# Kernel tuning notes

Measured on AMD Instinct MI355X. Metric: run time of the kernel, lower is better.

## Reference

```python
import jax, jax.numpy as jnp
import numpy as np

N = 20000; DX = 512; DW = 64; DY = 256; M = 320000
DS = DX // 2; DD = DX // 4; DP = DS + DD  # 256, 128, 384
EPS = 1e-9; LN_EPS = 1e-5; SLOPE = 0.05
PNAMES = ['rW1','rb1','rg1','rbt1','rW2','rb2','yW1','yb1','yg1','ybt1','yW2','yb2',
          'iaW1','iab1','iag1','iabt1','iaW2','iab2','cW1','cb1','cg1','cbt1','cW2','cb2']

def _mlp2(h, W1, b1, g, be, W2, b2):
    # Linear -> LayerNorm -> LeakyReLU(0.05) -> Linear  (matches mlp(..., norm='layer'))
    h = h @ W1 + b1
    mu = jnp.mean(h, axis=-1, keepdims=True)
    var = jnp.mean((h - mu) ** 2, axis=-1, keepdims=True)
    h = (h - mu) * jax.lax.rsqrt(var + LN_EPS) * g + be
    h = jnp.where(h >= 0, h, SLOPE * h)
    return h @ W2 + b2

def _m(Pp, n, h):
    return _mlp2(h, Pp[n+'W1'], Pp[n+'b1'], Pp[n+'g1'], Pp[n+'bt1'], Pp[n+'W2'], Pp[n+'b2'])

def _agg(a, b):
    s = a + b
    return jnp.where(s >= 0, s, SLOPE * s)

def _run(x, ei, edge_attr, u_r, u_ia, u_pick, Pp, dec=None):
    """GuoUnpool forward (steps 1a, 2a, 2b). ei: concrete numpy [2,M] int64.
    dec holds concrete sampled decisions; built from the uniforms when None."""
    build = dec is None
    if build:
        dec = {}
    # coalesce (edges are duplicate-free) + lexsort by (src, dst)
    perm = np.argsort(ei[0].astype(np.int64) * N + ei[1].astype(np.int64), kind='stable')
    src, dst = ei[0][perm], ei[1][perm]
    ea = edge_attr[perm]
    # --- step 1a: bernoulli unpool decision per node (I_s = I_u = empty, I_r = all nodes)
    pr = jax.nn.sigmoid(_m(Pp, 'r', x)[:, 0])
    if build:
        dec['choose'] = np.asarray(u_r) < np.asarray(pr)
    choose = dec['choose']
    Iu = np.flatnonzero(choose); Is = np.flatnonzero(~choose)
    logP = jnp.sum(jnp.where(jnp.asarray(choose), jnp.log(pr + EPS), jnp.log(1.0 - pr + EPS)))
    prs = jnp.clip(pr, EPS, 1.0 - EPS)
    ent = -jnp.sum(prs * jnp.log(prs) + (1.0 - prs) * jnp.log(1.0 - prs))
    # --- projections (_ps1_idx = [0:ds+D], _ps2_idx = [0:ds] + [ds+D:ds+2D]) and child embeddings
    ps1 = x[:, :DP]
    ps2 = jnp.concatenate([x[:, :DS], x[:, DS + DD:DS + 2 * DD]], axis=-1)
    y1 = _m(Pp, 'y', ps1)   # [N, dy]; rows at Is give x_static, rows at Iu give x_c1
    y2 = _m(Pp, 'y', ps2)   # rows at Iu give x_c2
    x_out = jnp.concatenate([y1[Is], y1[Iu], y2[Iu]], axis=0)
    # --- step 2a: intra-edge decision for unpooled nodes
    p_ia = jax.nn.sigmoid(_m(Pp, 'ia', _agg(y1[Iu], y2[Iu]))[:, 0])
    if build:
        dec['vc'] = np.asarray(u_ia)[Iu] < np.asarray(p_ia)
    vc = dec['vc']
    logP = logP + jnp.sum(jnp.where(jnp.asarray(vc), jnp.log(p_ia + EPS), jnp.log(1.0 - p_ia + EPS)))
    ps = jnp.clip(p_ia, EPS, 1.0 - EPS)
    ent = ent - jnp.sum(ps * jnp.log(ps) + (1.0 - ps) * jnp.log(1.0 - ps))
    # --- step 2b: categorical neighbor pick for unpooled nodes without intra edge
    if build:
        iun = Iu[~vc]
        par = np.concatenate([src, dst]); nb = np.concatenate([dst, src])
        ek = np.concatenate([np.arange(len(src)), np.arange(len(src))])
        keep = np.zeros(N, dtype=bool); keep[iun] = True
        msk = keep[par]
        par, nb, ek = par[msk], nb[msk], ek[msk]
        o = np.lexsort((nb, par))  # adj lists sorted by neighbor id, grouped by parent
        par, nb, ek = par[o], nb[o], ek[o]
        new = np.r_[True, par[1:] != par[:-1]]
        dec['par'], dec['nb'], dec['ek'] = par, nb, ek
        dec['seg'] = np.cumsum(new) - 1
        dec['starts'] = np.flatnonzero(new)
    par, nb, ek = dec['par'], dec['nb'], dec['ek']
    segn, starts = dec['seg'], dec['starts']
    Pn = len(par); nseg = int(segn[-1]) + 1
    seg = jnp.asarray(segn)
    yagg = _agg(y1, y2)
    feats = jnp.concatenate([yagg[par], ea[ek], x[nb]], axis=-1)  # [Pn, dy+dw+dx]
    scores = _m(Pp, 'c', feats)[:, 0]
    mx = jax.ops.segment_max(scores, seg, num_segments=nseg)
    e = jnp.exp(scores - mx[segn])
    den = jax.ops.segment_sum(e, seg, num_segments=nseg)
    probs = e / den[segn]                      # per-parent softmax over neighbors
    if build:
        # multinomial pick via inverse CDF on the provided per-parent uniform
        p_np = np.asarray(probs).astype(np.float64)
        cum = np.cumsum(p_np)
        base = np.concatenate([[0.0], cum])[starts]
        cumw = cum - base[segn]
        useg = np.asarray(u_pick)[par[starts]][segn]
        cand = np.where(cumw > useg, np.arange(Pn), Pn)
        pick = np.minimum.reduceat(cand, starts)
        last = np.r_[starts[1:] - 1, Pn - 1]
        dec['pick'] = np.minimum(pick, last)
    pick = dec['pick']
    logP = logP + jnp.sum(jnp.log(jnp.clip(probs[pick], EPS, None)))
    pc = jnp.clip(probs, EPS, None)
    ent = ent - jnp.sum(pc * jnp.log(pc))
    return (x_out, logP, ent), dec

def _init_params(key):
    Pp = {}
    specs = [('r', DX, max(1, DX // 2), 1), ('y', DP, 128, DY), ('ia', DY, 128, 1), ('c', DY + DW + DX, 128, 1)]
    ks = jax.random.split(key, len(specs))
    for (n, a, h, o), k in zip(specs, ks):
        k1, k2 = jax.random.split(k)
        Pp[n+'W1'] = jax.random.normal(k1, (a, h), jnp.float32) / np.sqrt(a)
        Pp[n+'b1'] = jnp.zeros((h,), jnp.float32)
        Pp[n+'g1'] = jnp.ones((h,), jnp.float32)
        Pp[n+'bt1'] = jnp.zeros((h,), jnp.float32)
        Pp[n+'W2'] = jax.random.normal(k2, (h, o), jnp.float32) / np.sqrt(h)
        Pp[n+'b2'] = jnp.zeros((o,), jnp.float32)
    return Pp

def setup_inputs() -> dict:
    key = jax.random.key(0)
    k = jax.random.split(key, 6)
    x = jax.random.normal(k[0], (N, DX), jnp.float32)
    rng = np.random.default_rng(0)
    ns = int(M * 1.5)
    s = rng.integers(0, N, ns); d = rng.integers(0, N, ns)
    ok = s != d; s, d = s[ok], d[ok]
    _, ui = np.unique(s.astype(np.int64) * N + d, return_index=True)  # duplicate-free (coalesced)
    sel = rng.permutation(ui)[:M]
    edge_index = jnp.asarray(np.stack([s[sel], d[sel]]).astype(np.int64))
    inp = {
        'x': x,
        'edge_index': edge_index,
        'edge_attr': 0.5 * jax.random.normal(k[1], (M, DW), jnp.float32),
        'u_r': jax.random.uniform(k[2], (N,), jnp.float32),
        'u_ia': jax.random.uniform(k[3], (N,), jnp.float32),
        'u_pick': jax.random.uniform(k[4], (N,), jnp.float32),
    }
    inp.update(_init_params(k[5]))
    return inp

def reference(x, edge_index, edge_attr, u_r, u_ia, u_pick,
              rW1, rb1, rg1, rbt1, rW2, rb2,
              yW1, yb1, yg1, ybt1, yW2, yb2,
              iaW1, iab1, iag1, iabt1, iaW2, iab2,
              cW1, cb1, cg1, cbt1, cW2, cb2):
    Pp = dict(zip(PNAMES, (rW1, rb1, rg1, rbt1, rW2, rb2, yW1, yb1, yg1, ybt1, yW2, yb2,
                           iaW1, iab1, iag1, iabt1, iaW2, iab2, cW1, cb1, cg1, cbt1, cW2, cb2)))
    out, _ = _run(x, np.asarray(edge_index), edge_attr, u_r, u_ia, u_pick, Pp)
    return out
```

## Files before the change

### kernel.cpp

```cpp
#include <hip/hip_runtime.h>
#include <math.h>

#define KN 20000
#define KM 320000

typedef __attribute__((ext_vector_type(8))) short bf16x8;
typedef __attribute__((ext_vector_type(4))) float f32x4;

__device__ __forceinline__ ushort f2bf(float f){
  union{float f; unsigned u;} a; a.f=f;
  unsigned r = a.u + 0x7FFFu + ((a.u>>16)&1u);
  return (ushort)(r>>16);
}
__device__ __forceinline__ float bf2f(ushort u){
  union{unsigned u; float f;} a; a.u=((unsigned)u)<<16; return a.f;
}

__device__ __forceinline__ void blk_add2(double lp, double en, double* acc, double* sh){
#pragma unroll
  for (int o=32;o;o>>=1){ lp+=__shfl_xor(lp,o,64); en+=__shfl_xor(en,o,64); }
  int w=threadIdx.x>>6;
  if ((threadIdx.x&63)==0){ sh[2*w]=lp; sh[2*w+1]=en; }
  __syncthreads();
  if (threadIdx.x==0){
    double L=0,E=0; int nw=(blockDim.x+63)>>6;
    for (int i=0;i<nw;i++){L+=sh[2*i];E+=sh[2*i+1];}
    atomicAdd(&acc[0],L); atomicAdd(&acc[1],E);
  }
  __syncthreads();
}

__global__ void k_init(int* __restrict__ deg,int* __restrict__ fill,int* __restrict__ keep,
                       int* __restrict__ counters,double* __restrict__ acc){
  int i=blockIdx.x*blockDim.x+threadIdx.x;
  if (i<KN){ deg[i]=0; fill[i]=0; keep[i]=0; }
  if (i<8) counters[i]=0;
  if (i<2) acc[i]=0.0;
}

__global__ __launch_bounds__(256) void k_cvt2(const float* __restrict__ src,
    ushort* __restrict__ hi, ushort* __restrict__ lo, int n8){
  int i=blockIdx.x*256+threadIdx.x;
  if (i<n8){
    const float* s=src+(size_t)i*8;
    union{ushort u[8]; uint4 v;} oh, ol;
#pragma unroll
    for (int j=0;j<8;j++){
      float v=s[j];
      ushort h=f2bf(v);
      oh.u[j]=h;
      ol.u[j]=f2bf(v-bf2f(h));
    }
    *(uint4*)(hi+(size_t)i*8)=oh.v;
    *(uint4*)(lo+(size_t)i*8)=ol.v;
  }
}

__global__ __launch_bounds__(256) void k_prep_w1d(const float* __restrict__ W1, double* __restrict__ w1d){
  int i=blockIdx.x*256+threadIdx.x;
  if (i<512*256) w1d[i]=(double)W1[i];
}
__global__ __launch_bounds__(256) void k_prep_wr2(const float* __restrict__ W1,
    ushort* __restrict__ Wrt_hi, ushort* __restrict__ Wrt_lo){
  int i=blockIdx.x*256+threadIdx.x;
  if (i<512*256){
    int n=i&255, k=i>>8;
    float wv=W1[(size_t)k*256+n];
    ushort h=f2bf(wv);
    int kt=k>>5, kc=(k>>3)&3, j=k&7;
    size_t dst=(((size_t)kt*1024)+(size_t)kc*256+(size_t)n)*8+j;
    Wrt_hi[dst]=h;
    Wrt_lo[dst]=f2bf(wv-bf2f(h));
  }
}

#define RFLAG_TAU 3e-4f
__global__ __launch_bounds__(512) void k_rmlp_fast2(const float* __restrict__ x,
    const ushort* __restrict__ x_hi,const ushort* __restrict__ x_lo,
    const ushort* __restrict__ Wrt_hi,const ushort* __restrict__ Wrt_lo,
    const double* __restrict__ w1d,
    const float* __restrict__ b1,const float* __restrict__ g1,
    const float* __restrict__ bt1,const float* __restrict__ W2,const float* __restrict__ b2,
    const float* __restrict__ u_r, float* __restrict__ pr, int* __restrict__ choose){
  __shared__ __align__(16) ushort Bl[2][2][8192];
  __shared__ float psum[64][2], pvar[64][2], pdot[64][2];
  __shared__ int flagsh[64];
  __shared__ double dsh[256];
  int t=threadIdx.x;
  int w=t>>6, l=t&63;
  int lr=l&15, lk=l>>4;
  int rg=w>>1, ch=w&1;
  int row0=blockIdx.x*64;
  if (t<64) flagsh[t]=0;
  int q0=t*2, q1=t*2+1;
  f32x4 acc[8];
#pragma unroll
  for (int c=0;c<8;c++) acc[c]=(f32x4){0,0,0,0};
  int rowA=row0+rg*16+lr; if (rowA>=KN) rowA=KN-1;
  const ushort* ah=x_hi+(size_t)rowA*512;
  const ushort* al=x_lo+(size_t)rowA*512;
  bf16x8 nh0=*(const bf16x8*)(Wrt_hi+q0*8);
  bf16x8 nh1=*(const bf16x8*)(Wrt_hi+q1*8);
  bf16x8 nl0=*(const bf16x8*)(Wrt_lo+q0*8);
  bf16x8 nl1=*(const bf16x8*)(Wrt_lo+q1*8);
  *(bf16x8*)&Bl[0][0][q0*8]=nh0; *(bf16x8*)&Bl[0][0][q1*8]=nh1;
  *(bf16x8*)&Bl[0][1][q0*8]=nl0; *(bf16x8*)&Bl[0][1][q1*8]=nl1;
  nh0=*(const bf16x8*)(Wrt_hi+8192+q0*8);
  nh1=*(const bf16x8*)(Wrt_hi+8192+q1*8);
  nl0=*(const bf16x8*)(Wrt_lo+8192+q0*8);
  nl1=*(const bf16x8*)(Wrt_lo+8192+q1*8);
  bf16x8 a_h0=*(const bf16x8*)(ah+0*32+lk*8), a_l0=*(const bf16x8*)(al+0*32+lk*8);
  bf16x8 a_h1=*(const bf16x8*)(ah+1*32+lk*8), a_l1=*(const bf16x8*)(al+1*32+lk*8);
  bf16x8 a_h2=*(const bf16x8*)(ah+2*32+lk*8), a_l2=*(const bf16x8*)(al+2*32+lk*8);
  bf16x8 a_h3=*(const bf16x8*)(ah+3*32+lk*8), a_l3=*(const bf16x8*)(al+3*32+lk*8);
  __syncthreads();
#define RBODY(KT,AH,AL) { \
    const int cur_=(KT)&1, nxt_=cur_^1; \
    if ((KT)<15){ \
      *(bf16x8*)&Bl[nxt_][0][q0*8]=nh0; *(bf16x8*)&Bl[nxt_][0][q1*8]=nh1; \
      *(bf16x8*)&Bl[nxt_][1][q0*8]=nl0; *(bf16x8*)&Bl[nxt_][1][q1*8]=nl1; \
      if ((KT)<14){ \
        size_t so_=(size_t)((KT)+2)*8192; \
        nh0=*(const bf16x8*)(Wrt_hi+so_+q0*8); nh1=*(const bf16x8*)(Wrt_hi+so_+q1*8); \
// ... 111 lines not shown
      for (int o=32;o;o>>=1) dot+=__shfl_xor(dot,o,64);
      if (t==0){
        double p=1.0/(1.0+exp(-(dot+(double)b2[0])));
        float pf=(float)p;
        pr[n]=pf;
        choose[n]=(u_r[n]<pf)?1:0;
      }
    }
    __syncthreads();
  }
}

__global__ __launch_bounds__(1024) void k_scan_choose(const int* __restrict__ choose,int* __restrict__ excl,
                                                      int* __restrict__ iu,int* __restrict__ counters){
  __shared__ int wsum[16], woff[16];
  const int CH=(KN+1023)/1024;
  int t=threadIdx.x, lane=t&63, wid=t>>6;
  int base=t*CH;
  int s=0;
  for (int i=0;i<CH;i++){int idx=base+i; if (idx<KN) s+=choose[idx];}
  int inc=s;
  for (int o=1;o<64;o<<=1){ int v=__shfl_up(inc,o,64); if (lane>=o) inc+=v; }
  if (lane==63) wsum[wid]=inc;
  __syncthreads();
  if (t==0){ int r=0; for (int i=0;i<16;i++){ woff[i]=r; r+=wsum[i]; } counters[2]=r; }
  __syncthreads();
  int ex=woff[wid]+inc-s;
  for (int i=0;i<CH;i++){
    int idx=base+i;
    if (idx<KN){ int c=choose[idx]; excl[idx]=ex; if (c) iu[ex]=idx; ex+=c; }
  }
}

__global__ void k_prep_w1yt(const float* __restrict__ W1, ushort* __restrict__ W1yt){
  int i=blockIdx.x*256+threadIdx.x;
  if (i<384*128){
    int n=i&127, k=i>>7;
    W1yt[(size_t)n*384+k]=f2bf(W1[(size_t)k*128+n]);
  }
}
__global__ void k_prep_w2yt(const float* __restrict__ W2, ushort* __restrict__ W2yt){
  int i=blockIdx.x*256+threadIdx.x;
  if (i<128*256){
    int n=i&255, k=i>>8;
    W2yt[(size_t)n*128+k]=f2bf(W2[(size_t)k*256+n]);
  }
}

#define YEXTP 261
__global__ __launch_bounds__(256) void k_ymlp_v2(const ushort* __restrict__ x_bf,
    const ushort* __restrict__ W1yt,const float* __restrict__ b1,const float* __restrict__ g1,
    const float* __restrict__ bt1,const ushort* __restrict__ W2yt,const float* __restrict__ b2,
    const int* __restrict__ choose,const int* __restrict__ excl,int cnt,
    float* __restrict__ yagg_f,ushort* __restrict__ yagg_bf,
    float* __restrict__ out){
  __shared__ __align__(16) char smem[16896+8704];
  float*  hf  =(float*)smem;
  float*  yext=(float*)smem;
  ushort* hb  =(ushort*)(smem+16896);
  int t=threadIdx.x;
  int w=t>>6, l=t&63;
  int lr=l&15, lk=l>>4;
  int md=w&1, kh=w>>1;
  int row0=blockIdx.x*16;
  f32x4 acc[8];
#pragma unroll
  for (int c=0;c<8;c++) acc[c]=(f32x4){0,0,0,0};
  const ushort* xr=x_bf+(size_t)(row0+lr)*512;
#pragma unroll
  for (int kt=0;kt<6;kt++){
    int k0=kh*192+kt*32+lk*8;
    int ks=(md && k0>=256)? k0+128 : k0;
    bf16x8 a=*(const bf16x8*)(xr+ks);
#pragma unroll
    for (int c=0;c<8;c++){
      bf16x8 b=*(const bf16x8*)(W1yt+(size_t)(c*16+lr)*384+k0);
      acc[c]=__builtin_amdgcn_mfma_f32_16x16x32_bf16(a,b,acc[c],0,0,0);
    }
  }
  if (kh==0){
#pragma unroll
    for (int i=0;i<4;i++){
      int row=lk*4+i;
#pragma unroll
      for (int c=0;c<8;c++) hf[((size_t)md*16+row)*132+c*16+lr]=acc[c][i];
    }
  }
  __syncthreads();
  if (kh==1){
    float b1v[8],g1v[8],btv[8];
#pragma unroll
    for (int c=0;c<8;c++){ int col=c*16+lr; b1v[c]=b1[col]; g1v[c]=g1[col]; btv[c]=bt1[col]; }
#pragma unroll
    for (int i=0;i<4;i++){
      int row=lk*4+i;
      float hv[8]; float s=0.f;
#pragma unroll
      for (int c=0;c<8;c++){ hv[c]=acc[c][i]+hf[((size_t)md*16+row)*132+c*16+lr]+b1v[c]; s+=hv[c]; }
#pragma unroll
      for (int o=8;o;o>>=1) s+=__shfl_xor(s,o,64);
      float mu=s*(1.0f/128.0f);
      float v=0.f;
#pragma unroll
      for (int c=0;c<8;c++){ float d=hv[c]-mu; v+=d*d; }
#pragma unroll
      for (int o=8;o;o>>=1) v+=__shfl_xor(v,o,64);
      float rs=1.0f/sqrtf(v*(1.0f/128.0f)+1e-5f);
      ushort* hrow=hb+((size_t)md*16+row)*136;
#pragma unroll
      for (int c=0;c<8;c++){
        float hn=(hv[c]-mu)*rs*g1v[c]+btv[c];
        hn=hn>=0.f?hn:0.05f*hn;
        hrow[c*16+lr]=f2bf(hn);
      }
    }
  }
  __syncthreads();
  f32x4 acc2[8];
#pragma unroll
  for (int c=0;c<8;c++) acc2[c]=(f32x4){0,0,0,0};
  const ushort* ha=hb+((size_t)md*16+lr)*136;
#pragma unroll
  for (int kt=0;kt<4;kt++){
    bf16x8 a=*(const bf16x8*)(ha+kt*32+lk*8);
#pragma unroll
    for (int c=0;c<8;c++){
      bf16x8 b=*(const bf16x8*)(W2yt+(size_t)(kh*128+c*16+lr)*128+kt*32+lk*8);
      acc2[c]=__builtin_amdgcn_mfma_f32_16x16x32_bf16(a,b,acc2[c],0,0,0);
    }
  }
  float b2v[8];
#pragma unroll
  for (int c=0;c<8;c++) b2v[c]=b2[kh*128+c*16+lr];
  if (md==0){
#pragma unroll
    for (int i=0;i<4;i++){
      int row=lk*4+i;
#pragma unroll
      for (int c=0;c<8;c++) yext[(size_t)row*YEXTP+kh*128+c*16+lr]=acc2[c][i]+b2v[c];
    }
  }
  __syncthreads();
  if (md==0){
#pragma unroll
    for (int i=0;i<4;i++){
      int row=lk*4+i, n=row0+row;
      int cch=choose[n], ex=excl[n];
      int r1 = cch? (KN-cnt)+ex : n-ex;
      if (r1>=0 && r1<KN+cnt){
        float* orow=out+(size_t)r1*256+kh*128;
#pragma unroll
        for (int c=0;c<8;c++) orow[c*16+lr]=acc2[c][i]+b2v[c];
      }
    }
  } else {
#pragma unroll
    for (int i=0;i<4;i++){
      int row=lk*4+i, n=row0+row;
      int cch=choose[n], ex=excl[n];
      size_t base=(size_t)n*256+kh*128;
#pragma unroll
      for (int c=0;c<8;c++){
        int colk=c*16+lr;
        float v2=acc2[c][i]+b2v[c];
        float v1=yext[(size_t)row*YEXTP+kh*128+colk];
        float ga=v1+v2; ga=ga>=0.f?ga:0.05f*ga;
        yagg_f[base+colk]=ga;
        yagg_bf[base+colk]=f2bf(ga);
        if (cch){ int r2=KN+ex; if (r2<KN+cnt) out[(size_t)r2*256+kh*128+colk]=v2; }
      }
    }
  }
}

__global__ __launch_bounds__(256) void k_node_term(const float* __restrict__ pr,const int* __restrict__ choose,
                                                   double* __restrict__ acc){
  __shared__ double sh[8];
  int i=blockIdx.x*256+threadIdx.x;
  double lp=0,en=0;
  if (i<KN){
    double p=(double)pr[i];
    lp = choose[i]? log(p+1e-9) : log(1.0-p+1e-9);
    double ps=fmin(fmax(p,1e-9),1.0-1e-9);
    en = -(ps*log(ps)+(1.0-ps)*log(1.0-ps));
  }
  blk_add2(lp,en,acc,sh);
}

__global__ __launch_bounds__(128) void k_ia(const float* __restrict__ yagg_f,
    const int* __restrict__ iu,const float* __restrict__ u_ia,
    const float* __restrict__ W1,const float* __restrict__ b1,const float* __restrict__ g1,
    const float* __restrict__ bt1,const float* __restrict__ W2,const float* __restrict__ b2,
    float* __restrict__ p_ia,int* __restrict__ vc,int* __restrict__ keep,double* __restrict__ acc,int cnt){
  __shared__ float insh[8][256];
  __shared__ float hsh[8][128];
  __shared__ double sh[8];
  int t=threadIdx.x;
  int row0=blockIdx.x*8;
  for (int i=t;i<8*256;i+=128){
    int r=i>>8,k=i&255;
    int row=row0+r;
    if (row<cnt){
      unsigned n=(unsigned)iu[row];
      if (n<KN) insh[r][k]=yagg_f[(size_t)n*256+k];
      else insh[r][k]=0.f;
    }
  }
  __syncthreads();
  float accv[8]; float bb=b1[t];
#pragma unroll
  for (int r=0;r<8;r++) accv[r]=bb;
  for (int k=0;k<256;k+=4){
    float w0=W1[(k+0)*128+t],w1=W1[(k+1)*128+t],w2=W1[(k+2)*128+t],w3=W1[(k+3)*128+t];
#pragma unroll
    for (int r=0;r<8;r++){
      float4 f=*(const float4*)&insh[r][k];
      accv[r]=fmaf(f.x,w0,accv[r]); accv[r]=fmaf(f.y,w1,accv[r]); accv[r]=fmaf(f.z,w2,accv[r]); accv[r]=fmaf(f.w,w3,accv[r]);
    }
  }
#pragma unroll
  for (int r=0;r<8;r++) hsh[r][t]=accv[r];
  __syncthreads();
  int g=t>>4, tl=t&15;
  float hv[8];
#pragma unroll
  for (int j=0;j<8;j++) hv[j]=hsh[g][tl+16*j];
  float s=0;
#pragma unroll
  for (int j=0;j<8;j++) s+=hv[j];
#pragma unroll
  for (int o=8;o;o>>=1) s+=__shfl_xor(s,o,64);
  float mu=s*(1.0f/128.0f);
  float v=0;
#pragma unroll
  for (int j=0;j<8;j++){float d=hv[j]-mu; v+=d*d;}
#pragma unroll
  for (int o=8;o;o>>=1) v+=__shfl_xor(v,o,64);
  float rs=1.0f/sqrtf(v*(1.0f/128.0f)+1e-5f);
  float dot=0;
#pragma unroll
  for (int j=0;j<8;j++){
    int idx=tl+16*j;
    float hn=(hv[j]-mu)*rs*g1[idx]+bt1[idx];
    hn=hn>=0.f?hn:0.05f*hn;
    dot=fmaf(hn,W2[idx],dot);
  }
#pragma unroll
  for (int o=8;o;o>>=1) dot+=__shfl_xor(dot,o,64);
  double lp=0,en=0;
  if (tl==0){
    int row=row0+g;
    if (row<cnt){
      unsigned n=(unsigned)iu[row];
      if (n<KN){
// ... 41 lines not shown
  __syncthreads();
  int inc2=sc;
  for (int o=1;o<64;o<<=1){ int v=__shfl_up(inc2,o,64); if (lane>=o) inc2+=v; }
  if (lane==63) wsum[wid]=inc2;
  __syncthreads();
  if (t==0){ int r=0; for (int i=0;i<16;i++){ woff[i]=r; r+=wsum[i]; } counters[1]=r; }
  __syncthreads();
  int ex2=woff[wid]+inc2-sc;
  for (int i=0;i<CH;i++){int idx=base+i; if(idx<KN && deg[idx]>0){ nodeseg[ex2]=idx; ex2++; }}
}

__global__ void k_fill(const int* __restrict__ ei,const int* __restrict__ keep,const int* __restrict__ boff,
                       int* __restrict__ fill,int* __restrict__ parA,int* __restrict__ keyA,int* __restrict__ ekA){
  int e=blockIdx.x*256+threadIdx.x;
  if (e<KM){
    int s=ei[e], d=ei[KM+e];
    if (keep[s]){ int pos=boff[s]+atomicAdd(&fill[s],1); parA[pos]=s; keyA[pos]=d*2;   ekA[pos]=e; }
    if (keep[d]){ int pos=boff[d]+atomicAdd(&fill[d],1); parA[pos]=d; keyA[pos]=s*2+1; ekA[pos]=e; }
  }
}

__global__ void k_rank(const int* __restrict__ parA,const int* __restrict__ keyA,const int* __restrict__ ekA,
                       const int* __restrict__ boff,const int* __restrict__ counters,
                       int* __restrict__ parS,int* __restrict__ nbS,int* __restrict__ ekS){
  int i=blockIdx.x*256+threadIdx.x;
  int Pn=counters[0];
  if (i<Pn){
    int par=parA[i], key=keyA[i];
    int lo=boff[par], hi=boff[par+1];
    int rank=0;
    for (int j=lo;j<hi;j++) rank += (keyA[j]<key)?1:0;
    int pos=lo+rank;
    parS[pos]=par; nbS[pos]=key>>1; ekS[pos]=ekA[i];
  }
}

__global__ void k_prep_w1t(const float* __restrict__ W1, ushort* __restrict__ W1t){
  int i=blockIdx.x*256+threadIdx.x;
  if (i<832*128){
    int n=i&127, k=i>>7;
    W1t[(size_t)n*832+k]=f2bf(W1[(size_t)k*128+n]);
  }
}

__global__ __launch_bounds__(256) void k_hpre_v3(const ushort* __restrict__ yagg_bf,
    const ushort* __restrict__ x_bf,const ushort* __restrict__ W1t,
    float* __restrict__ hyP,float* __restrict__ hxP){
  int t=threadIdx.x;
  int w=t>>6, l=t&63;
  int lr=l&15, lk=l>>4;
  int row0=blockIdx.x*16;
  int cq=w&1;
  f32x4 acc[4];
#pragma unroll
  for (int c=0;c<4;c++) acc[c]=(f32x4){0,0,0,0};
  if (w<2){
    const ushort* ar=yagg_bf+(size_t)(row0+lr)*256+lk*8;
#pragma unroll
    for (int kt=0;kt<8;kt++){
      bf16x8 a=*(const bf16x8*)(ar+kt*32);
#pragma unroll
      for (int c=0;c<4;c++){
        bf16x8 b=*(const bf16x8*)(W1t+(size_t)(cq*64+c*16+lr)*832+kt*32+lk*8);
        acc[c]=__builtin_amdgcn_mfma_f32_16x16x32_bf16(a,b,acc[c],0,0,0);
      }
    }
#pragma unroll
    for (int i=0;i<4;i++){
      int n=row0+lk*4+i;
      float4 v; v.x=acc[0][i]; v.y=acc[1][i]; v.z=acc[2][i]; v.w=acc[3][i];
      *(float4*)(hyP+(size_t)n*128+lr*8+cq*4)=v;
    }
  } else {
    const ushort* ar=x_bf+(size_t)(row0+lr)*512+lk*8;
#pragma unroll
    for (int kt=0;kt<16;kt++){
      bf16x8 a=*(const bf16x8*)(ar+kt*32);
#pragma unroll
      for (int c=0;c<4;c++){
        bf16x8 b=*(const bf16x8*)(W1t+(size_t)(cq*64+c*16+lr)*832+320+kt*32+lk*8);
        acc[c]=__builtin_amdgcn_mfma_f32_16x16x32_bf16(a,b,acc[c],0,0,0);
      }
    }
#pragma unroll
    for (int i=0;i<4;i++){
      int n=row0+lk*4+i;
      float4 v; v.x=acc[0][i]; v.y=acc[1][i]; v.z=acc[2][i]; v.w=acc[3][i];
      *(float4*)(hxP+(size_t)n*128+lr*8+cq*4)=v;
    }
  }
}

__global__ __launch_bounds__(256) void k_cscore_v6(
    const float* __restrict__ ea,const float* __restrict__ hyP,const float* __restrict__ hxP,
    const int* __restrict__ parS,const int* __restrict__ nbS,const int* __restrict__ ekS,
    const int* __restrict__ counters,
    const ushort* __restrict__ W1t,const float* __restrict__ b1,const float* __restrict__ g1,
    const float* __restrict__ bt1,const float* __restrict__ W2,const float* __restrict__ b2,
    float* __restrict__ scores){
  int Pn=counters[0];
  if (Pn<=0) return;
  int t=threadIdx.x;
  int w=t>>6, l=t&63;
  int lr=l&15, lk=l>>4;
  float b2s=b2[0];
  float b1v[8],g1v[8],btv[8],w2v[8];
#pragma unroll
  for (int c=0;c<8;c++){
    int col=c*16+lr;
    b1v[c]=b1[col]; g1v[c]=g1[col]; btv[c]=bt1[col]; w2v[c]=W2[col];
  }
  int ngrp=(Pn+63)>>6;
  for (int g=blockIdx.x; g<ngrp; g+=gridDim.x){
    int p0=g*64+w*16;
    float hs[4][8];
#pragma unroll
    for (int i=0;i<4;i++){
      int p=p0+lk*4+i; int pc=p<Pn?p:Pn-1;
      const float* hyp=hyP+(size_t)parS[pc]*128+lr*8;
      const float* hxp=hxP+(size_t)nbS[pc]*128+lr*8;
      float4 ya=*(const float4*)hyp, yb=*(const float4*)(hyp+4);
      float4 xa=*(const float4*)hxp, xb=*(const float4*)(hxp+4);
// ... 97 lines not shown
  const float* u_r   =(const float*)d_in[3];
  const float* u_ia  =(const float*)d_in[4];
  const float* u_pick=(const float*)d_in[5];
  const float* Pp[24];
  for (int i=0;i<24;i++) Pp[i]=(const float*)d_in[6+i];
  float* out=(float*)d_out;
  int cnt=(out_size-2)/256 - KN;
  if (cnt<0) cnt=0;

  char* w=(char*)d_ws;
  size_t off=0;
  auto carve=[&](size_t bytes)->char*{ off=(off+255)&~(size_t)255; char* p=w+off; off+=bytes; return p; };
  int*    counters=(int*)   carve(64);
  double* acc     =(double*)carve(64);
  float*  pr      =(float*) carve((size_t)KN*4);
  int*    choose  =(int*)   carve((size_t)KN*4);
  int*    excl    =(int*)   carve((size_t)KN*4);
  int*    iu      =(int*)   carve((size_t)KN*4);
  float*  p_ia    =(float*) carve((size_t)KN*4);
  int*    vc      =(int*)   carve((size_t)KN*4);
  int*    keep    =(int*)   carve((size_t)KN*4);
  int*    deg     =(int*)   carve((size_t)KN*4);
  int*    fill    =(int*)   carve((size_t)KN*4);
  int*    boff    =(int*)   carve((size_t)(KN+1)*4);
  int*    nodeseg =(int*)   carve((size_t)KN*4);
  int*    parA    =(int*)   carve((size_t)2*KM*4);
  int*    keyA    =(int*)   carve((size_t)2*KM*4);
  int*    ekA     =(int*)   carve((size_t)2*KM*4);
  int*    parS    =(int*)   carve((size_t)2*KM*4);
  int*    nbS     =(int*)   carve((size_t)2*KM*4);
  int*    ekS     =(int*)   carve((size_t)2*KM*4);
  float*  scores  =(float*) carve((size_t)2*KM*4);
  float*  yagg_f  =(float*) carve((size_t)KN*256*4);
  ushort* yagg_bf =(ushort*)carve((size_t)KN*256*2);
  ushort* x_bf    =(ushort*)carve((size_t)KN*512*2);
  ushort* x_lo    =(ushort*)carve((size_t)KN*512*2);
  ushort* W1t     =(ushort*)carve((size_t)832*128*2);
  double* w1d     =(double*)carve((size_t)512*256*8);
  ushort* W1yt    =(ushort*)carve((size_t)128*384*2);
  ushort* W2yt    =(ushort*)carve((size_t)256*128*2);
  ushort* Wrt_hi  =(ushort*)carve((size_t)256*512*2);
  ushort* Wrt_lo  =(ushort*)carve((size_t)256*512*2);
  float*  hy      =(float*) carve((size_t)KN*128*4);
  float*  hx      =(float*) carve((size_t)KN*128*4);
  (void)ws_size;(void)n_in;(void)in_sizes;

  k_init<<<(KN+255)/256,256,0,stream>>>(deg,fill,keep,counters,acc);
  k_prep_w1t<<<(832*128+255)/256,256,0,stream>>>(Pp[18],W1t);
  k_prep_w1yt<<<(384*128+255)/256,256,0,stream>>>(Pp[6],W1yt);
  k_prep_w2yt<<<(128*256+255)/256,256,0,stream>>>(Pp[10],W2yt);
  k_prep_wr2<<<(512*256+255)/256,256,0,stream>>>(Pp[0],Wrt_hi,Wrt_lo);
  k_prep_w1d<<<(512*256+255)/256,256,0,stream>>>(Pp[0],w1d);
  k_cvt2<<<(KN*512/8+255)/256,256,0,stream>>>(x,x_bf,x_lo,KN*512/8);
  k_rmlp_fast2<<<(KN+63)/64,512,0,stream>>>(x,x_bf,x_lo,Wrt_hi,Wrt_lo,w1d,
      Pp[1],Pp[2],Pp[3],Pp[4],Pp[5],u_r,pr,choose);
  k_scan_choose<<<1,1024,0,stream>>>(choose,excl,iu,counters);
  k_ymlp_v2<<<KN/16,256,0,stream>>>(x_bf,W1yt,Pp[7],Pp[8],Pp[9],W2yt,Pp[11],choose,excl,cnt,yagg_f,yagg_bf,out);
  k_hpre_v3<<<KN/16,256,0,stream>>>(yagg_bf,x_bf,W1t,hy,hx);
  k_node_term<<<(KN+255)/256,256,0,stream>>>(pr,choose,acc);
  if (cnt>0)
    k_ia<<<(cnt+7)/8,128,0,stream>>>(yagg_f,iu,u_ia,Pp[12],Pp[13],Pp[14],Pp[15],Pp[16],Pp[17],p_ia,vc,keep,acc,cnt);
  k_count<<<(KM+255)/256,256,0,stream>>>(ei,keep,deg);
  k_scan_deg<<<1,1024,0,stream>>>(deg,boff,nodeseg,counters);
  k_fill<<<(KM+255)/256,256,0,stream>>>(ei,keep,boff,fill,parA,keyA,ekA);
  k_rank<<<(2*KM+255)/256,256,0,stream>>>(parA,keyA,ekA,boff,counters,parS,nbS,ekS);
  k_cscore_v6<<<2560,256,0,stream>>>(ea,hy,hx,parS,nbS,ekS,counters,W1t,Pp[19],Pp[20],Pp[21],Pp[22],Pp[23],scores);
  k_segment<<<(KN+255)/256,256,0,stream>>>(scores,boff,nodeseg,counters,u_pick,acc);
  k_final<<<1,64,0,stream>>>(acc,out,cnt);
}
```

Baseline: 460.8 us.

## Fuse hy/hx pre-projection GEMMs into the y-MLP kernel

Moves the cW1 pre-projection work of k_hpre_v3 into the end of the y-MLP kernel. The bf16 aggregated y rows now stay in shared memory instead of being written to and reread from a global yagg_bf buffer, and one kernel launch is removed. Each of the four waves computes 32 output columns for both the x and y parts. The cost is extra shared memory and a longer kernel with an added barrier, which may lower occupancy.

```diff
diff --git a/kernel.cpp b/kernel.cpp
--- a/kernel.cpp
+++ b/kernel.cpp
@@ -282,25 +282,28 @@
 }
 
 #define YEXTP 261
-__global__ __launch_bounds__(256) void k_ymlp_v2(const ushort* __restrict__ x_bf,
+#define YBP 264
+__global__ __launch_bounds__(256) void k_ymlp_v3(const ushort* __restrict__ x_bf,
     const ushort* __restrict__ W1yt,const float* __restrict__ b1,const float* __restrict__ g1,
     const float* __restrict__ bt1,const ushort* __restrict__ W2yt,const float* __restrict__ b2,
+    const ushort* __restrict__ W1t,
     const int* __restrict__ choose,const int* __restrict__ excl,int cnt,
-    float* __restrict__ yagg_f,ushort* __restrict__ yagg_bf,
+    float* __restrict__ yagg_f,float* __restrict__ hyP,float* __restrict__ hxP,
     float* __restrict__ out){
-  __shared__ __align__(16) char smem[16896+8704];
+  __shared__ __align__(16) char smem[16896+8704+16*YBP*2];
   float*  hf  =(float*)smem;
   float*  yext=(float*)smem;
   ushort* hb  =(ushort*)(smem+16896);
+  ushort* yb  =(ushort*)(smem+16896+8704);
   int t=threadIdx.x;
   int w=t>>6, l=t&63;
   int lr=l&15, lk=l>>4;
   int md=w&1, kh=w>>1;
   int row0=blockIdx.x*16;
+  const ushort* xr=x_bf+(size_t)(row0+lr)*512;
   f32x4 acc[8];
 #pragma unroll
   for (int c=0;c<8;c++) acc[c]=(f32x4){0,0,0,0};
-  const ushort* xr=x_bf+(size_t)(row0+lr)*512;
 #pragma unroll
   for (int kt=0;kt<6;kt++){
     int k0=kh*192+kt*32+lk*8;
@@ -361,6 +364,26 @@
     for (int c=0;c<8;c++){
       bf16x8 b=*(const bf16x8*)(W2yt+(size_t)(kh*128+c*16+lr)*128+kt*32+lk*8);
       acc2[c]=__builtin_amdgcn_mfma_f32_16x16x32_bf16(a,b,acc2[c],0,0,0);
+    }
+  }
+  {
+    f32x4 acc3[2];
+#pragma unroll
+    for (int c=0;c<2;c++) acc3[c]=(f32x4){0,0,0,0};
+#pragma unroll
+    for (int kt=0;kt<16;kt++){
+      bf16x8 a=*(const bf16x8*)(xr+320+kt*32+lk*8);
+#pragma unroll
+      for (int c=0;c<2;c++){
+        bf16x8 b=*(const bf16x8*)(W1t+(size_t)(w*32+c*16+lr)*832+320+kt*32+lk*8);
+        acc3[c]=__builtin_amdgcn_mfma_f32_16x16x32_bf16(a,b,acc3[c],0,0,0);
+      }
+    }
+#pragma unroll
+    for (int i=0;i<4;i++){
+      int n=row0+lk*4+i;
+      float2 v; v.x=acc3[0][i]; v.y=acc3[1][i];
+      *(float2*)(hxP+(size_t)n*128+lr*8+w*2)=v;
     }
   }
   float b2v[8];
@@ -400,9 +423,30 @@
         float v1=yext[(size_t)row*YEXTP+kh*128+colk];
         float ga=v1+v2; ga=ga>=0.f?ga:0.05f*ga;
         yagg_f[base+colk]=ga;
-        yagg_bf[base+colk]=f2bf(ga);
+        yb[(size_t)row*YBP+kh*128+colk]=f2bf(ga);
         if (cch){ int r2=KN+ex; if (r2<KN+cnt) out[(size_t)r2*256+kh*128+colk]=v2; }
       }
+    }
+  }
+  __syncthreads();
+  {
+    f32x4 acc4[2];
+#pragma unroll
+    for (int c=0;c<2;c++) acc4[c]=(f32x4){0,0,0,0};
+#pragma unroll
+    for (int kt=0;kt<8;kt++){
+      bf16x8 a=*(const bf16x8*)&yb[(size_t)lr*YBP+kt*32+lk*8];
+#pragma unroll
+      for (int c=0;c<2;c++){
+        bf16x8 b=*(const bf16x8*)(W1t+(size_t)(w*32+c*16+lr)*832+kt*32+lk*8);
+        acc4[c]=__builtin_amdgcn_mfma_f32_16x16x32_bf16(a,b,acc4[c],0,0,0);
+      }
+    }
+#pragma unroll
+    for (int i=0;i<4;i++){
+      int n=row0+lk*4+i;
+      float2 v; v.x=acc4[0][i]; v.y=acc4[1][i];
+      *(float2*)(hyP+(size_t)n*128+lr*8+w*2)=v;
     }
   }
 }
@@ -569,54 +613,6 @@
   if (i<832*128){
     int n=i&127, k=i>>7;
     W1t[(size_t)n*832+k]=f2bf(W1[(size_t)k*128+n]);
-  }
-}
-
-__global__ __launch_bounds__(256) void k_hpre_v3(const ushort* __restrict__ yagg_bf,
-    const ushort* __restrict__ x_bf,const ushort* __restrict__ W1t,
-    float* __restrict__ hyP,float* __restrict__ hxP){
-  int t=threadIdx.x;
-  int w=t>>6, l=t&63;
-  int lr=l&15, lk=l>>4;
-  int row0=blockIdx.x*16;
-  int cq=w&1;
-  f32x4 acc[4];
-#pragma unroll
-  for (int c=0;c<4;c++) acc[c]=(f32x4){0,0,0,0};
-  if (w<2){
-    const ushort* ar=yagg_bf+(size_t)(row0+lr)*256+lk*8;
-#pragma unroll
-    for (int kt=0;kt<8;kt++){
-      bf16x8 a=*(const bf16x8*)(ar+kt*32);
-#pragma unroll
-      for (int c=0;c<4;c++){
-        bf16x8 b=*(const bf16x8*)(W1t+(size_t)(cq*64+c*16+lr)*832+kt*32+lk*8);
-        acc[c]=__builtin_amdgcn_mfma_f32_16x16x32_bf16(a,b,acc[c],0,0,0);
-      }
-    }
-#pragma unroll
-    for (int i=0;i<4;i++){
-      int n=row0+lk*4+i;
-      float4 v; v.x=acc[0][i]; v.y=acc[1][i]; v.z=acc[2][i]; v.w=acc[3][i];
-      *(float4*)(hyP+(size_t)n*128+lr*8+cq*4)=v;
-    }
-  } else {
-    const ushort* ar=x_bf+(size_t)(row0+lr)*512+lk*8;
-#pragma unroll
-    for (int kt=0;kt<16;kt++){
-      bf16x8 a=*(const bf16x8*)(ar+kt*32);
-#pragma unroll
-      for (int c=0;c<4;c++){
-        bf16x8 b=*(const bf16x8*)(W1t+(size_t)(cq*64+c*16+lr)*832+320+kt*32+lk*8);
-        acc[c]=__builtin_amdgcn_mfma_f32_16x16x32_bf16(a,b,acc[c],0,0,0);
-      }
-    }
-#pragma unroll
-    for (int i=0;i<4;i++){
-      int n=row0+lk*4+i;
-      float4 v; v.x=acc[0][i]; v.y=acc[1][i]; v.z=acc[2][i]; v.w=acc[3][i];
-      *(float4*)(hxP+(size_t)n*128+lr*8+cq*4)=v;
-    }
   }
 }
 
@@ -780,7 +776,6 @@
   int*    ekS     =(int*)   carve((size_t)2*KM*4);
   float*  scores  =(float*) carve((size_t)2*KM*4);
   float*  yagg_f  =(float*) carve((size_t)KN*256*4);
-  ushort* yagg_bf =(ushort*)carve((size_t)KN*256*2);
   ushort* x_bf    =(ushort*)carve((size_t)KN*512*2);
   ushort* x_lo    =(ushort*)carve((size_t)KN*512*2);
   ushort* W1t     =(ushort*)carve((size_t)832*128*2);
@@ -803,8 +798,8 @@
   k_rmlp_fast2<<<(KN+63)/64,512,0,stream>>>(x,x_bf,x_lo,Wrt_hi,Wrt_lo,w1d,
       Pp[1],Pp[2],Pp[3],Pp[4],Pp[5],u_r,pr,choose);
   k_scan_choose<<<1,1024,0,stream>>>(choose,excl,iu,counters);
-  k_ymlp_v2<<<KN/16,256,0,stream>>>(x_bf,W1yt,Pp[7],Pp[8],Pp[9],W2yt,Pp[11],choose,excl,cnt,yagg_f,yagg_bf,out);
-  k_hpre_v3<<<KN/16,256,0,stream>>>(yagg_bf,x_bf,W1t,hy,hx);
+  k_ymlp_v3<<<KN/16,256,0,stream>>>(x_bf,W1yt,Pp[7],Pp[8],Pp[9],W2yt,Pp[11],W1t,
+      choose,excl,cnt,yagg_f,hy,hx,out);
   k_node_term<<<(KN+255)/256,256,0,stream>>>(pr,choose,acc);
   if (cnt>0)
     k_ia<<<(cnt+7)/8,128,0,stream>>>(yagg_f,iu,u_ia,Pp[12],Pp[13],Pp[14],Pp[15],Pp[16],Pp[17],p_ia,vc,keep,acc,cnt);
```

Result: no change. 462.1 us (+0.3%).

## Merge prep kernels and co-schedule independent GEMMs as extra blocks in launches

Applied to the files above, without the earlier changes.

Folds the seven init and weight-prep kernels into one k_prep_all launch. Moves the hx projection into extra blocks of the r-MLP kernel, the node log-prob/entropy reduction into extra blocks of the y-MLP kernel, and the hy projection into extra blocks of the ia kernel, which now also handles 16 rows per block. This cuts launch count and lets independent work fill idle CUs alongside the main kernels. In exchange the combined kernels carry the larger shared-memory and register footprint of the heaviest branch, which may lower occupancy for the lighter blocks.

```diff
diff --git a/kernel.cpp b/kernel.cpp
--- a/kernel.cpp
+++ b/kernel.cpp
@@ -30,19 +30,18 @@
   __syncthreads();
 }
 
-__global__ void k_init(int* __restrict__ deg,int* __restrict__ fill,int* __restrict__ keep,
-                       int* __restrict__ counters,double* __restrict__ acc){
-  int i=blockIdx.x*blockDim.x+threadIdx.x;
-  if (i<KN){ deg[i]=0; fill[i]=0; keep[i]=0; }
-  if (i<8) counters[i]=0;
-  if (i<2) acc[i]=0.0;
-}
-
-__global__ __launch_bounds__(256) void k_cvt2(const float* __restrict__ src,
-    ushort* __restrict__ hi, ushort* __restrict__ lo, int n8){
+__global__ __launch_bounds__(256) void k_prep_all(
+    const float* __restrict__ x, ushort* __restrict__ x_hi, ushort* __restrict__ x_lo,
+    const float* __restrict__ Wr1, ushort* __restrict__ Wrt_hi, ushort* __restrict__ Wrt_lo,
+    double* __restrict__ w1d,
+    const float* __restrict__ Wc1, ushort* __restrict__ W1t,
+    const float* __restrict__ Wy1, ushort* __restrict__ W1yt,
+    const float* __restrict__ Wy2, ushort* __restrict__ W2yt,
+    int* __restrict__ deg,int* __restrict__ fill,int* __restrict__ keep,
+    int* __restrict__ counters,double* __restrict__ acc){
   int i=blockIdx.x*256+threadIdx.x;
-  if (i<n8){
-    const float* s=src+(size_t)i*8;
+  if (i<KN*512/8){
+    const float* s=x+(size_t)i*8;
     union{ushort u[8]; uint4 v;} oh, ol;
 #pragma unroll
     for (int j=0;j<8;j++){
@@ -51,37 +50,45 @@
       oh.u[j]=h;
       ol.u[j]=f2bf(v-bf2f(h));
     }
-    *(uint4*)(hi+(size_t)i*8)=oh.v;
-    *(uint4*)(lo+(size_t)i*8)=ol.v;
-  }
-}
-
-__global__ __launch_bounds__(256) void k_prep_w1d(const float* __restrict__ W1, double* __restrict__ w1d){
-  int i=blockIdx.x*256+threadIdx.x;
-  if (i<512*256) w1d[i]=(double)W1[i];
-}
-__global__ __launch_bounds__(256) void k_prep_wr2(const float* __restrict__ W1,
-    ushort* __restrict__ Wrt_hi, ushort* __restrict__ Wrt_lo){
-  int i=blockIdx.x*256+threadIdx.x;
+    *(uint4*)(x_hi+(size_t)i*8)=oh.v;
+    *(uint4*)(x_lo+(size_t)i*8)=ol.v;
+  }
   if (i<512*256){
+    w1d[i]=(double)Wr1[i];
     int n=i&255, k=i>>8;
-    float wv=W1[(size_t)k*256+n];
+    float wv=Wr1[(size_t)k*256+n];
     ushort h=f2bf(wv);
     int kt=k>>5, kc=(k>>3)&3, j=k&7;
     size_t dst=(((size_t)kt*1024)+(size_t)kc*256+(size_t)n)*8+j;
     Wrt_hi[dst]=h;
     Wrt_lo[dst]=f2bf(wv-bf2f(h));
   }
+  if (i<832*128){
+    int n=i&127, k=i>>7;
+    W1t[(size_t)n*832+k]=f2bf(Wc1[(size_t)k*128+n]);
+  }
+  if (i<384*128){
+    int n=i&127, k=i>>7;
+    W1yt[(size_t)n*384+k]=f2bf(Wy1[(size_t)k*128+n]);
+  }
+  if (i<128*256){
+    int n=i&255, k=i>>8;
+    W2yt[(size_t)n*128+k]=f2bf(Wy2[(size_t)k*256+n]);
+  }
+  if (i<KN){ deg[i]=0; fill[i]=0; keep[i]=0; }
+  if (i<8) counters[i]=0;
+  if (i<2) acc[i]=0.0;
 }
 
 #define RFLAG_TAU 3e-4f
-__global__ __launch_bounds__(512) void k_rmlp_fast2(const float* __restrict__ x,
+__global__ __launch_bounds__(512) void k_rmlp_hx(const float* __restrict__ x,
     const ushort* __restrict__ x_hi,const ushort* __restrict__ x_lo,
     const ushort* __restrict__ Wrt_hi,const ushort* __restrict__ Wrt_lo,
     const double* __restrict__ w1d,
     const float* __restrict__ b1,const float* __restrict__ g1,
     const float* __restrict__ bt1,const float* __restrict__ W2,const float* __restrict__ b2,
-    const float* __restrict__ u_r, float* __restrict__ pr, int* __restrict__ choose){
+    const float* __restrict__ u_r, float* __restrict__ pr, int* __restrict__ choose,
+    const ushort* __restrict__ W1t, float* __restrict__ hxP, int RB){
   __shared__ __align__(16) ushort Bl[2][2][8192];
   __shared__ float psum[64][2], pvar[64][2], pdot[64][2];
   __shared__ int flagsh[64];
@@ -89,6 +96,31 @@
   int t=threadIdx.x;
   int w=t>>6, l=t&63;
   int lr=l&15, lk=l>>4;
+  if ((int)blockIdx.x>=RB){
+    int b2=blockIdx.x-RB;
+    int rh=w>>2, cw=w&3;
+    int row0=b2*32+rh*16;
+    const ushort* ar=x_hi+(size_t)(row0+lr)*512;
+    f32x4 acc3[2];
+#pragma unroll
+    for (int c=0;c<2;c++) acc3[c]=(f32x4){0,0,0,0};
+#pragma unroll
+    for (int kt=0;kt<16;kt++){
+      bf16x8 a=*(const bf16x8*)(ar+320+kt*32+lk*8);
+#pragma unroll
+      for (int c=0;c<2;c++){
+        bf16x8 b=*(const bf16x8*)(W1t+(size_t)(cw*32+c*16+lr)*832+320+kt*32+lk*8);
+        acc3[c]=__builtin_amdgcn_mfma_f32_16x16x32_bf16(a,b,acc3[c],0,0,0);
+      }
+    }
+#pragma unroll
+    for (int i=0;i<4;i++){
+      int n=row0+lk*4+i;
+      float2 v; v.x=acc3[0][i]; v.y=acc3[1][i];
+      *(float2*)(hxP+(size_t)n*128+lr*8+cw*2)=v;
+    }
+    return;
+  }
   int rg=w>>1, ch=w&1;
   int row0=blockIdx.x*64;
   if (t<64) flagsh[t]=0;
@@ -266,40 +298,39 @@
   }
 }
 
-__global__ void k_prep_w1yt(const float* __restrict__ W1, ushort* __restrict__ W1yt){
-  int i=blockIdx.x*256+threadIdx.x;
-  if (i<384*128){
-    int n=i&127, k=i>>7;
-    W1yt[(size_t)n*384+k]=f2bf(W1[(size_t)k*128+n]);
-  }
-}
-__global__ void k_prep_w2yt(const float* __restrict__ W2, ushort* __restrict__ W2yt){
-  int i=blockIdx.x*256+threadIdx.x;
-  if (i<128*256){
-    int n=i&255, k=i>>8;
-    W2yt[(size_t)n*128+k]=f2bf(W2[(size_t)k*256+n]);
-  }
-}
-
 #define YEXTP 261
-__global__ __launch_bounds__(256) void k_ymlp_v2(const ushort* __restrict__ x_bf,
+__global__ __launch_bounds__(256) void k_ymlp_nt(const ushort* __restrict__ x_bf,
     const ushort* __restrict__ W1yt,const float* __restrict__ b1,const float* __restrict__ g1,
     const float* __restrict__ bt1,const ushort* __restrict__ W2yt,const float* __restrict__ b2,
     const int* __restrict__ choose,const int* __restrict__ excl,int cnt,
     float* __restrict__ yagg_f,ushort* __restrict__ yagg_bf,
-    float* __restrict__ out){
+    float* __restrict__ out,
+    const float* __restrict__ pr,double* __restrict__ acc,int YB){
   __shared__ __align__(16) char smem[16896+8704];
+  int t=threadIdx.x;
+  if ((int)blockIdx.x>=YB){
+    double* sh=(double*)smem;
+    int i=(blockIdx.x-YB)*256+t;
+    double lp=0,en=0;
+    if (i<KN){
+      double p=(double)pr[i];
+      lp = choose[i]? log(p+1e-9) : log(1.0-p+1e-9);
+      double ps=fmin(fmax(p,1e-9),1.0-1e-9);
+      en = -(ps*log(ps)+(1.0-ps)*log(1.0-ps));
+    }
+    blk_add2(lp,en,acc,sh);
+    return;
+  }
   float*  hf  =(float*)smem;
   float*  yext=(float*)smem;
   ushort* hb  =(ushort*)(smem+16896);
-  int t=threadIdx.x;
   int w=t>>6, l=t&63;
   int lr=l&15, lk=l>>4;
   int md=w&1, kh=w>>1;
   int row0=blockIdx.x*16;
-  f32x4 acc[8];
-#pragma unroll
-  for (int c=0;c<8;c++) acc[c]=(f32x4){0,0,0,0};
+  f32x4 acc1[8];
+#pragma unroll
+  for (int c=0;c<8;c++) acc1[c]=(f32x4){0,0,0,0};
   const ushort* xr=x_bf+(size_t)(row0+lr)*512;
 #pragma unroll
   for (int kt=0;kt<6;kt++){
@@ -309,7 +340,7 @@
 #pragma unroll
     for (int c=0;c<8;c++){
       bf16x8 b=*(const bf16x8*)(W1yt+(size_t)(c*16+lr)*384+k0);
-      acc[c]=__builtin_amdgcn_mfma_f32_16x16x32_bf16(a,b,acc[c],0,0,0);
+      acc1[c]=__builtin_amdgcn_mfma_f32_16x16x32_bf16(a,b,acc1[c],0,0,0);
     }
   }
   if (kh==0){
@@ -317,7 +348,7 @@
     for (int i=0;i<4;i++){
       int row=lk*4+i;
 #pragma unroll
-      for (int c=0;c<8;c++) hf[((size_t)md*16+row)*132+c*16+lr]=acc[c][i];
+      for (int c=0;c<8;c++) hf[((size_t)md*16+row)*132+c*16+lr]=acc1[c][i];
     }
   }
   __syncthreads();
@@ -330,7 +361,7 @@
       int row=lk*4+i;
       float hv[8]; float s=0.f;
 #pragma unroll
-      for (int c=0;c<8;c++){ hv[c]=acc[c][i]+hf[((size_t)md*16+row)*132+c*16+lr]+b1v[c]; s+=hv[c]; }
+      for (int c=0;c<8;c++){ hv[c]=acc1[c][i]+hf[((size_t)md*16+row)*132+c*16+lr]+b1v[c]; s+=hv[c]; }
 #pragma unroll
       for (int o=8;o;o>>=1) s+=__shfl_xor(s,o,64);
       float mu=s*(1.0f/128.0f);
@@ -407,31 +438,45 @@
   }
 }
 
-__global__ __launch_bounds__(256) void k_node_term(const float* __restrict__ pr,const int* __restrict__ choose,
-                                                   double* __restrict__ acc){
-  __shared__ double sh[8];
-  int i=blockIdx.x*256+threadIdx.x;
-  double lp=0,en=0;
-  if (i<KN){
-    double p=(double)pr[i];
-    lp = choose[i]? log(p+1e-9) : log(1.0-p+1e-9);
-    double ps=fmin(fmax(p,1e-9),1.0-1e-9);
-    en = -(ps*log(ps)+(1.0-ps)*log(1.0-ps));
-  }
-  blk_add2(lp,en,acc,sh);
-}
-
-__global__ __launch_bounds__(128) void k_ia(const float* __restrict__ yagg_f,
+__global__ __launch_bounds__(256) void k_ia_hy(const float* __restrict__ yagg_f,
+    const ushort* __restrict__ yagg_bf,const ushort* __restrict__ W1t,float* __restrict__ hyP,
     const int* __restrict__ iu,const float* __restrict__ u_ia,
     const float* __restrict__ W1,const float* __restrict__ b1,const float* __restrict__ g1,
     const float* __restrict__ bt1,const float* __restrict__ W2,const float* __restrict__ b2,
-    float* __restrict__ p_ia,int* __restrict__ vc,int* __restrict__ keep,double* __restrict__ acc,int cnt){
-  __shared__ float insh[8][256];
-  __shared__ float hsh[8][128];
+    float* __restrict__ p_ia,int* __restrict__ vc,int* __restrict__ keep,double* __restrict__ acc,
+    int cnt,int HB){
+  __shared__ float insh[16][256];
+  __shared__ float hsh[16][128];
   __shared__ double sh[8];
   int t=threadIdx.x;
-  int row0=blockIdx.x*8;
-  for (int i=t;i<8*256;i+=128){
+  int w=t>>6, l=t&63;
+  int lr=l&15, lk=l>>4;
+  if ((int)blockIdx.x<HB){
+    int rh=w>>1, cq=w&1;
+    int row0=blockIdx.x*32+rh*16;
+    const ushort* ar=yagg_bf+(size_t)(row0+lr)*256+lk*8;
+    f32x4 acc4[4];
+#pragma unroll
+    for (int c=0;c<4;c++) acc4[c]=(f32x4){0,0,0,0};
+#pragma unroll
+    for (int kt=0;kt<8;kt++){
+      bf16x8 a=*(const bf16x8*)(ar+kt*32);
+#pragma unroll
+      for (int c=0;c<4;c++){
+        bf16x8 b=*(const bf16x8*)(W1t+(size_t)(cq*64+c*16+lr)*832+kt*32+lk*8);
+        acc4[c]=__builtin_amdgcn_mfma_f32_16x16x32_bf16(a,b,acc4[c],0,0,0);
+      }
+    }
+#pragma unroll
+    for (int i=0;i<4;i++){
+      int n=row0+lk*4+i;
+      float4 v; v.x=acc4[0][i]; v.y=acc4[1][i]; v.z=acc4[2][i]; v.w=acc4[3][i];
+      *(float4*)(hyP+(size_t)n*128+lr*8+cq*4)=v;
+    }
+    return;
+  }
+  int row0=(blockIdx.x-HB)*16;
+  for (int i=t;i<16*256;i+=256){
     int r=i>>8,k=i&255;
     int row=row0+r;
     if (row<cnt){
@@ -441,19 +486,20 @@
     }
   }
   __syncthreads();
-  float accv[8]; float bb=b1[t];
+  int h=t>>7, tt=t&127;
+  float accv[8]; float bb=b1[tt];
 #pragma unroll
   for (int r=0;r<8;r++) accv[r]=bb;
   for (int k=0;k<256;k+=4){
-    float w0=W1[(k+0)*128+t],w1=W1[(k+1)*128+t],w2=W1[(k+2)*128+t],w3=W1[(k+3)*128+t];
+    float w0=W1[(k+0)*128+tt],w1=W1[(k+1)*128+tt],w2=W1[(k+2)*128+tt],w3=W1[(k+3)*128+tt];
 #pragma unroll
     for (int r=0;r<8;r++){
-      float4 f=*(const float4*)&insh[r][k];
+      float4 f=*(const float4*)&insh[h*8+r][k];
       accv[r]=fmaf(f.x,w0,accv[r]); accv[r]=fmaf(f.y,w1,accv[r]); accv[r]=fmaf(f.z,w2,accv[r]); accv[r]=fmaf(f.w,w3,accv[r]);
     }
   }
 #pragma unroll
-  for (int r=0;r<8;r++) hsh[r][t]=accv[r];
+  for (int r=0;r<8;r++) hsh[h*8+r][tt]=accv[r];
   __syncthreads();
   int g=t>>4, tl=t&15;
   float hv[8];
@@ -561,62 +607,6 @@
     for (int j=lo;j<hi;j++) rank += (keyA[j]<key)?1:0;
     int pos=lo+rank;
     parS[pos]=par; nbS[pos]=key>>1; ekS[pos]=ekA[i];
-  }
-}
-
-__global__ void k_prep_w1t(const float* __restrict__ W1, ushort* __restrict__ W1t){
-  int i=blockIdx.x*256+threadIdx.x;
-  if (i<832*128){
-    int n=i&127, k=i>>7;
-    W1t[(size_t)n*832+k]=f2bf(W1[(size_t)k*128+n]);
-  }
-}
-
-__global__ __launch_bounds__(256) void k_hpre_v3(const ushort* __restrict__ yagg_bf,
-    const ushort* __restrict__ x_bf,const ushort* __restrict__ W1t,
-    float* __restrict__ hyP,float* __restrict__ hxP){
-  int t=threadIdx.x;
-  int w=t>>6, l=t&63;
-  int lr=l&15, lk=l>>4;
-  int row0=blockIdx.x*16;
-  int cq=w&1;
-  f32x4 acc[4];
-#pragma unroll
-  for (int c=0;c<4;c++) acc[c]=(f32x4){0,0,0,0};
-  if (w<2){
-    const ushort* ar=yagg_bf+(size_t)(row0+lr)*256+lk*8;
-#pragma unroll
-    for (int kt=0;kt<8;kt++){
-      bf16x8 a=*(const bf16x8*)(ar+kt*32);
-#pragma unroll
-      for (int c=0;c<4;c++){
-        bf16x8 b=*(const bf16x8*)(W1t+(size_t)(cq*64+c*16+lr)*832+kt*32+lk*8);
-        acc[c]=__builtin_amdgcn_mfma_f32_16x16x32_bf16(a,b,acc[c],0,0,0);
-      }
-    }
-#pragma unroll
-    for (int i=0;i<4;i++){
-      int n=row0+lk*4+i;
-      float4 v; v.x=acc[0][i]; v.y=acc[1][i]; v.z=acc[2][i]; v.w=acc[3][i];
-      *(float4*)(hyP+(size_t)n*128+lr*8+cq*4)=v;
-    }
-  } else {
-    const ushort* ar=x_bf+(size_t)(row0+lr)*512+lk*8;
-#pragma unroll
-    for (int kt=0;kt<16;kt++){
-      bf16x8 a=*(const bf16x8*)(ar+kt*32);
-#pragma unroll
-      for (int c=0;c<4;c++){
-        bf16x8 b=*(const bf16x8*)(W1t+(size_t)(cq*64+c*16+lr)*832+320+kt*32+lk*8);
-        acc[c]=__builtin_amdgcn_mfma_f32_16x16x32_bf16(a,b,acc[c],0,0,0);
-      }
-    }
-#pragma unroll
-    for (int i=0;i<4;i++){
-      int n=row0+lk*4+i;
-      float4 v; v.x=acc[0][i]; v.y=acc[1][i]; v.z=acc[2][i]; v.w=acc[3][i];
-      *(float4*)(hxP+(size_t)n*128+lr*8+cq*4)=v;
-    }
   }
 }
 
@@ -793,21 +783,23 @@
   float*  hx      =(float*) carve((size_t)KN*128*4);
   (void)ws_size;(void)n_in;(void)in_sizes;
 
-  k_init<<<(KN+255)/256,256,0,stream>>>(deg,fill,keep,counters,acc);
-  k_prep_w1t<<<(832*128+255)/256,256,0,stream>>>(Pp[18],W1t);
-  k_prep_w1yt<<<(384*128+255)/256,256,0,stream>>>(Pp[6],W1yt);
-  k_prep_w2yt<<<(128*256+255)/256,256,0,stream>>>(Pp[10],W2yt);
-  k_prep_wr2<<<(512*256+255)/256,256,0,stream>>>(Pp[0],Wrt_hi,Wrt_lo);
-  k_prep_w1d<<<(512*256+255)/256,256,0,stream>>>(Pp[0],w1d);
-  k_cvt2<<<(KN*512/8+255)/256,256,0,stream>>>(x,x_bf,x_lo,KN*512/8);
-  k_rmlp_fast2<<<(KN+63)/64,512,0,stream>>>(x,x_bf,x_lo,Wrt_hi,Wrt_lo,w1d,
-      Pp[1],Pp[2],Pp[3],Pp[4],Pp[5],u_r,pr,choose);
+  const int RB=(KN+63)/64;
+  const int HXB=KN/32;
+  const int YB=KN/16;
+  const int NTB=(KN+255)/256;
+  const int HB=KN/32;
+  const int IAB=(cnt+15)/16;
+
+  k_prep_all<<<(KN*512/8+255)/256,256,0,stream>>>(x,x_bf,x_lo,
+      Pp[0],Wrt_hi,Wrt_lo,w1d, Pp[18],W1t, Pp[6],W1yt, Pp[10],W2yt,
+      deg,fill,keep,counters,acc);
+  k_rmlp_hx<<<RB+HXB,512,0,stream>>>(x,x_bf,x_lo,Wrt_hi,Wrt_lo,w1d,
+      Pp[1],Pp[2],Pp[3],Pp[4],Pp[5],u_r,pr,choose,W1t,hx,RB);
   k_scan_choose<<<1,1024,0,stream>>>(choose,excl,iu,counters);
-  k_ymlp_v2<<<KN/16,256,0,stream>>>(x_bf,W1yt,Pp[7],Pp[8],Pp[9],W2yt,Pp[11],choose,excl,cnt,yagg_f,yagg_bf,out);
-  k_hpre_v3<<<KN/16,256,0,stream>>>(yagg_bf,x_bf,W1t,hy,hx);
-  k_node_term<<<(KN+255)/256,256,0,stream>>>(pr,choose,acc);
-  if (cnt>0)
-    k_ia<<<(cnt+7)/8,128,0,stream>>>(yagg_f,iu,u_ia,Pp[12],Pp[13],Pp[14],Pp[15],Pp[16],Pp[17],p_ia,vc,keep,acc,cnt);
+  k_ymlp_nt<<<YB+NTB,256,0,stream>>>(x_bf,W1yt,Pp[7],Pp[8],Pp[9],W2yt,Pp[11],
+      choose,excl,cnt,yagg_f,yagg_bf,out,pr,acc,YB);
+  k_ia_hy<<<HB+IAB,256,0,stream>>>(yagg_f,yagg_bf,W1t,hy,iu,u_ia,
+      Pp[12],Pp[13],Pp[14],Pp[15],Pp[16],Pp[17],p_ia,vc,keep,acc,cnt,HB);
   k_count<<<(KM+255)/256,256,0,stream>>>(ei,keep,deg);
   k_scan_deg<<<1,1024,0,stream>>>(deg,boff,nodeseg,counters);
   k_fill<<<(KM+255)/256,256,0,stream>>>(ei,keep,boff,fill,parA,keyA,ekA);
```

Result: faster. 413.9 us (-10.2%).
